# Kernel tuning notes

Hardware: AMD Instinct MI355X
Metric: run time of the kernel (lower is better)

Reference implementation:

```python
import jax, jax.numpy as jnp
import numpy as np

NUM_HEADS = 16
HEAD_DIM = 96          # dim=1536 / 16 heads
ROPE_HALF = HEAD_DIM // 2   # 48 rotary frequencies
FREQ_PER_AXIS = ROPE_HALF // 3  # 16 frequencies per 3D coordinate axis
ROPE_BASE = 10000.0


def _rope_sincos(coords):
    # coords: [B, T, 3] -> sin, cos: [B, T, ROPE_HALF]
    inv_freq = 1.0 / (ROPE_BASE ** (jnp.arange(FREQ_PER_AXIS, dtype=jnp.float32) / FREQ_PER_AXIS))
    # angles per axis: [B, T, 3, F] -> concat axes -> [B, T, 3*F]
    ang = coords[..., :, None] * inv_freq  # [B, T, 3, F]
    ang = ang.reshape(*coords.shape[:-1], ROPE_HALF)
    return jnp.sin(ang), jnp.cos(ang)


def _apply_rotary(x, sin, cos):
    # x: [B, H, T, D]; sin/cos: [B, T, D/2] broadcast over heads
    s = sin[:, None, :, :]
    c = cos[:, None, :, :]
    x1, x2 = x[..., :ROPE_HALF], x[..., ROPE_HALF:]
    return jnp.concatenate([x1 * c - x2 * s, x2 * c + x1 * s], axis=-1)


def setup_inputs() -> dict:
    key = jax.random.key(0)
    ks = jax.random.split(key, 8)
    B, Tq, Tk, D = 2, 1024, 2048, 1536
    std = 1.0 / np.sqrt(D)
    return {
        "x": jax.random.normal(ks[0], (B, Tq, D), jnp.float32),
        "memory": jax.random.normal(ks[1], (B, Tk, D), jnp.float32),
        "query_coords": jax.random.normal(ks[2], (B, Tq, 3), jnp.float32),
        "memory_coords": jax.random.normal(ks[3], (B, Tk, 3), jnp.float32),
        "Wq": jax.random.normal(ks[4], (D, D), jnp.float32) * std,
        "bq": jnp.zeros((D,), jnp.float32),
        "Wk": jax.random.normal(ks[5], (D, D), jnp.float32) * std,
        "bk": jnp.zeros((D,), jnp.float32),
        "Wv": jax.random.normal(ks[6], (D, D), jnp.float32) * std,
        "bv": jnp.zeros((D,), jnp.float32),
        "Wo": jax.random.normal(ks[7], (D, D), jnp.float32) * std,
        "bo": jnp.zeros((D,), jnp.float32),
    }


def reference(x, memory, query_coords, memory_coords, Wq, bq, Wk, bk, Wv, bv, Wo, bo):
    B, Tq, D = x.shape
    Tk = memory.shape[1]
    H, Hd = NUM_HEADS, HEAD_DIM

    # projections (nn.Linear: y = x @ W^T + b)
    q = (jnp.einsum('btd,ed->bte', x, Wq) + bq).reshape(B, Tq, H, Hd).transpose(0, 2, 1, 3)
    k = (jnp.einsum('btd,ed->bte', memory, Wk) + bk).reshape(B, Tk, H, Hd).transpose(0, 2, 1, 3)
    v = (jnp.einsum('btd,ed->bte', memory, Wv) + bv).reshape(B, Tk, H, Hd).transpose(0, 2, 1, 3)

    # 3D-coordinate RoPE (identity augmentation: shift=0, jitter=1, rescale=1)
    q_sin, q_cos = _rope_sincos(query_coords)
    k_sin, k_cos = _rope_sincos(memory_coords)
    q = _apply_rotary(q, q_sin, q_cos)
    k = _apply_rotary(k, k_sin, k_cos)

    # SDPA (standard scaling): softmax(q k^T / sqrt(Hd)) v
    scale = 1.0 / jnp.sqrt(jnp.asarray(Hd, jnp.float32))
    scores = jnp.einsum('bhqd,bhkd->bhqk', q, k) * scale
    attn = jax.nn.softmax(scores, axis=-1)
    out = jnp.einsum('bhqk,bhkd->bhqd', attn, v)  # [B, H, Tq, Hd]

    out = out.transpose(0, 2, 1, 3).reshape(B, Tq, D)
    return jnp.einsum('btd,ed->bte', out, Wo) + bo
```

## Files before the change

### kernel.cpp

```cpp
#include <hip/hip_runtime.h>
#include <math.h>

typedef _Float16 f16;
typedef __attribute__((ext_vector_type(4))) _Float16 f16x4;
typedef __attribute__((ext_vector_type(8))) _Float16 f16x8;
typedef __attribute__((ext_vector_type(4))) float f32x4;
typedef __attribute__((ext_vector_type(16))) float f32x16;

#define NB 2
#define NH 16
#define TQ 1024
#define TK 2048
#define DM 1536
#define HD 96
#define RH 48

__device__ __forceinline__ f32x4 mfma16(f16x8 a, f16x8 b, f32x4 c) {
    return __builtin_amdgcn_mfma_f32_16x16x32_f16(a, b, c, 0, 0, 0);
}

#define GLDS16(gptr, lptr) __builtin_amdgcn_global_load_lds( \
    (const __attribute__((address_space(1))) unsigned int*)(gptr), \
    (__attribute__((address_space(3))) unsigned int*)(lptr), 16, 0, 0)

__global__ void cvt6(const float4* __restrict__ Wq, const float4* __restrict__ Wk,
                     const float4* __restrict__ Wv, const float4* __restrict__ Wo,
                     const float4* __restrict__ X,  const float4* __restrict__ M,
                     f16x4* __restrict__ oq, f16x4* __restrict__ ok,
                     f16x4* __restrict__ ov, f16x4* __restrict__ oo,
                     f16x4* __restrict__ ox, f16x4* __restrict__ om,
                     int nw4, int nx4, int nm4) {
    int i = blockIdx.x * 256 + threadIdx.x;
    const int y = blockIdx.y;
    const int n = (y < 4) ? nw4 : (y == 4 ? nx4 : nm4);
    if (i >= n) return;
    const float4* in = y == 0 ? Wq : y == 1 ? Wk : y == 2 ? Wv : y == 3 ? Wo : y == 4 ? X : M;
    f16x4* out      = y == 0 ? oq : y == 1 ? ok : y == 2 ? ov : y == 3 ? oo : y == 4 ? ox : om;
    float4 v = in[i];
    f16x4 o;
    o[0] = (f16)v.x; o[1] = (f16)v.y; o[2] = (f16)v.z; o[3] = (f16)v.w;
    out[i] = o;
}

__global__ void rope_tab2(const float* __restrict__ cq, const float* __restrict__ cm,
                          float* __restrict__ sq, float* __restrict__ cqo,
                          float* __restrict__ sk, float* __restrict__ cko,
                          int nq, int nk) {
    int i = blockIdx.x * 256 + threadIdx.x;
    int n = blockIdx.y == 0 ? nq : nk;
    if (i >= n) return;
    const float* coords = blockIdx.y == 0 ? cq : cm;
    float* sinT = blockIdx.y == 0 ? sq : sk;
    float* cosT = blockIdx.y == 0 ? cqo : cko;
    int bt = i / 48, idx = i - bt * 48;
    int axis = idx >> 4, f = idx & 15;
    float inv = powf(10000.f, -(float)f * (1.f / 16.f));
    float ang = coords[bt * 3 + axis] * inv;
    sinT[i] = sinf(ang);
    cosT[i] = cosf(ang);
}

__global__ void ropek4(f16* __restrict__ qk, const float* __restrict__ sinT,
                       const float* __restrict__ cosT, int n) {
    int i = blockIdx.x * 256 + threadIdx.x;
    if (i >= n) return;
    int j = i % 12, row = i / 12;
    int p0 = j * 4;
    int t = row & (TK - 1);
    int b = row / (NH * TK);
    long base = (long)row * 128;
    float4 sv = *(const float4*)&sinT[((long)b * TK + t) * 48 + p0];
    float4 cv = *(const float4*)&cosT[((long)b * TK + t) * 48 + p0];
    f16x4 x1 = *(const f16x4*)&qk[base + p0];
    f16x4 x2 = *(const f16x4*)&qk[base + p0 + RH];
    f16x4 o1, o2;
    float s[4] = {sv.x, sv.y, sv.z, sv.w}, c[4] = {cv.x, cv.y, cv.z, cv.w};
#pragma unroll
    for (int e = 0; e < 4; e++) {
        float a = (float)x1[e], bb = (float)x2[e];
        o1[e] = (f16)(a * c[e] - bb * s[e]);
        o2[e] = (f16)(bb * c[e] + a * s[e]);
    }
    *(f16x4*)&qk[base + p0] = o1;
    *(f16x4*)&qk[base + p0 + RH] = o2;
}

__global__ __launch_bounds__(512, 1)
void gemmQKV(const f16* __restrict__ Aq, const f16* __restrict__ Akv,
             const f16* __restrict__ Wqp, const f16* __restrict__ Wkp, const f16* __restrict__ Wvp,
             const float* __restrict__ bqp, const float* __restrict__ bkp, const float* __restrict__ bvp,
             f16* __restrict__ outq, f16* __restrict__ outk, f16* __restrict__ outv) {
    constexpr int MI = 8, NI = 4;
    constexpr int NT = DM / 64;

    __shared__ f16 Buf[2][256 * 64];

    const int tid = threadIdx.x, w = tid >> 6, lane = tid & 63;
    const int l15 = lane & 15, g = lane >> 4;

    int sel = 0, mt, nt;
    const f16* A; const f16* W; const float* bias;
    {
        const int bid = blockIdx.x;
        const int wid = (bid & 7) * 30 + (bid >> 3);
        if (wid < 48)       { sel = 0; mt = wid / 6;        nt = wid - mt * 6;        A = Aq;  W = Wqp; bias = bqp; }
        else if (wid < 144) { sel = 1; int r = wid - 48;  mt = r / 6; nt = r - mt * 6; A = Akv; W = Wkp; bias = bkp; }
        else                { sel = 2; int r = wid - 144; mt = r / 6; nt = r - mt * 6; A = Akv; W = Wvp; bias = bvp; }
    }
    const int m0 = mt * 256, n0 = nt * 256;
    const int wm = (w & 1) * 128;
    const int wn = (w >> 1) * 64;

    int src[4];
#pragma unroll
    for (int r = 0; r < 4; r++) {
        int L = r * 8192 + tid * 16;
        int row = L >> 7, seg = (L >> 4) & 7;
        src[r] = row * DM + ((seg ^ (row & 7)) << 3);
    }
    const f16* Ag = A + (long)m0 * DM;

    int aoff[MI][2];
#pragma unroll
    for (int i = 0; i < MI; i++) {
        int row = wm + i * 16 + l15;
#pragma unroll
        for (int s = 0; s < 2; s++)
            aoff[i][s] = row * 64 + (((s * 4 + g) ^ (row & 7)) << 3);
    }

    const f16* bptr[NI];
#pragma unroll
    for (int j = 0; j < NI; j++)
        bptr[j] = W + (long)(n0 + wn + j * 16 + l15) * DM + g * 8;

#define STG(bufp, kt) do { \
    _Pragma("unroll") for (int r_ = 0; r_ < 4; r_++) \
        GLDS16(Ag + src[r_] + (kt) * 64, &Buf[bufp][r_ * 4096 + w * 512]); \
} while (0)

#define LDB(breg, kt) do { \
    _Pragma("unroll") for (int j_ = 0; j_ < NI; j_++) \
        _Pragma("unroll") for (int s_ = 0; s_ < 2; s_++) \
            breg[j_][s_] = *(const f16x8*)(bptr[j_] + (kt) * 64 + s_ * 32); \
} while (0)

    f32x4 acc[MI][NI] = {};

#define COMPUTE(bufp, breg) do { \
    __builtin_amdgcn_s_setprio(1); \
    _Pragma("unroll") for (int i_ = 0; i_ < MI; i_++) { \
        f16x8 a0 = *(const f16x8*)&Buf[bufp][aoff[i_][0]]; \
        f16x8 a1 = *(const f16x8*)&Buf[bufp][aoff[i_][1]]; \
        _Pragma("unroll") for (int j_ = 0; j_ < NI; j_++) { \
            acc[i_][j_] = mfma16(a0, breg[j_][0], acc[i_][j_]); \
            acc[i_][j_] = mfma16(a1, breg[j_][1], acc[i_][j_]); \
        } \
    } \
    __builtin_amdgcn_s_setprio(0); \
} while (0)

    f16x8 bA[NI][2], bB[NI][2];
    STG(0, 0);
    LDB(bA, 0);

#pragma unroll 1
    for (int t = 0; t < NT; t += 2) {
        if (t + 1 < NT) {
            STG(1, t + 1);
            LDB(bB, t + 1);
            asm volatile("s_waitcnt vmcnt(12)" ::: "memory");
        } else {
            asm volatile("s_waitcnt vmcnt(0)" ::: "memory");
        }
        __builtin_amdgcn_s_barrier();
        __builtin_amdgcn_sched_barrier(0);
        COMPUTE(0, bA);
        __builtin_amdgcn_sched_barrier(0);
        __builtin_amdgcn_s_barrier();
        if (t + 2 < NT) {
            STG(0, t + 2);
            LDB(bA, t + 2);
            asm volatile("s_waitcnt vmcnt(12)" ::: "memory");
        } else {
            asm volatile("s_waitcnt vmcnt(0)" ::: "memory");
        }
        __builtin_amdgcn_s_barrier();
        __builtin_amdgcn_sched_barrier(0);
        COMPUTE(1, bB);
        __builtin_amdgcn_sched_barrier(0);
        __builtin_amdgcn_s_barrier();
    }
#undef STG
#undef LDB
#undef COMPUTE

#pragma unroll
    for (int i = 0; i < MI; i++) {
#pragma unroll
        for (int j = 0; j < NI; j++) {
            const int n = n0 + wn + j * 16 + l15;
            const int mb = m0 + wm + i * 16 + g * 4;
            const int hh = n / HD, hd = n - hh * HD;
            if (sel == 0) {
#pragma unroll
                for (int r = 0; r < 4; r++) {
                    int m = mb + r, bq = m >> 10, t = m & (TQ - 1);
                    outq[(((long)bq * NH + hh) * TQ + t) * 96 + hd] = (f16)(acc[i][j][r] + bias[n]);
                }
            } else if (sel == 1) {
#pragma unroll
                for (int r = 0; r < 4; r++) {
                    int m = mb + r, bq = m >> 11, t = m & (TK - 1);
                    outk[(((long)bq * NH + hh) * TK + t) * 128 + hd] = (f16)(acc[i][j][r] + bias[n]);
                }
            } else {
                int bq = mb >> 11, t = mb & (TK - 1);
                f16x4 pk;
#pragma unroll
                for (int r = 0; r < 4; r++) pk[r] = (f16)(acc[i][j][r] + bias[n]);
                *(f16x4*)&outv[(((long)bq * NH + hh) * HD + hd) * TK + t] = pk;
            }
        }
    }
}

__global__ __launch_bounds__(256, 2)
void gemmO(const f16* __restrict__ A, const f16* __restrict__ W,
           const float* __restrict__ bias, float* __restrict__ outo) {
    constexpr int TPB = 256, MI = 4, NI = 4;
    constexpr int ABUF = 128 * 64;
    constexpr int BUFSZ = 256 * 64;
    constexpr int NT = DM / 64;

    __shared__ f16 Buf[2][BUFSZ];

    const int tid = threadIdx.x, w = tid >> 6, lane = tid & 63;
    const int l15 = lane & 15, g = lane >> 4;
    const int bid = blockIdx.x;
    const int wid = (bid & 7) * 24 + (bid >> 3);
    const int mt = wid / 12, nt = wid - mt * 12;
    const int m0 = mt * 128, n0 = nt * 128;
    const int wm = (w & 1) * 64;
    const int wn = (w >> 1) * 64;

    int src[4];
#pragma unroll
    for (int r = 0; r < 4; r++) {
        int L = r * (TPB * 16) + tid * 16;
        int row = L >> 7, seg = (L >> 4) & 7;
        src[r] = row * DM + ((seg ^ (row & 7)) << 3);
    }
    const f16* Ag = A + (long)m0 * DM;
    const f16* Bg = W + (long)n0 * DM;

    int aoff[MI][2], boff[NI][2];
#pragma unroll
    for (int i = 0; i < MI; i++) {
        int row = wm + i * 16 + l15;
#pragma unroll
        for (int s = 0; s < 2; s++)
            aoff[i][s] = row * 64 + (((s * 4 + g) ^ (row & 7)) << 3);
    }
#pragma unroll
    for (int j = 0; j < NI; j++) {
        int row = wn + j * 16 + l15;
#pragma unroll
        for (int s = 0; s < 2; s++)
            boff[j][s] = ABUF + row * 64 + (((s * 4 + g) ^ (row & 7)) << 3);
    }

#define STG(bufp, kt) do { \
    _Pragma("unroll") for (int r_ = 0; r_ < 4; r_++) { \
        GLDS16(Ag + src[r_] + (kt) * 64, &Buf[bufp][r_ * (TPB * 8) + w * 512]); \
        GLDS16(Bg + src[r_] + (kt) * 64, &Buf[bufp][ABUF + r_ * (TPB * 8) + w * 512]); \
    } \
} while (0)

    f32x4 acc[MI][NI] = {};

#define COMPUTE(bufp) do { \
    f16x8 bf[NI][2]; \
    _Pragma("unroll") for (int j_ = 0; j_ < NI; j_++) \
        _Pragma("unroll") for (int s_ = 0; s_ < 2; s_++) \
            bf[j_][s_] = *(const f16x8*)&Buf[bufp][boff[j_][s_]]; \
    __builtin_amdgcn_s_setprio(1); \
    _Pragma("unroll") for (int i_ = 0; i_ < MI; i_++) { \
        f16x8 a0 = *(const f16x8*)&Buf[bufp][aoff[i_][0]]; \
        f16x8 a1 = *(const f16x8*)&Buf[bufp][aoff[i_][1]]; \
        _Pragma("unroll") for (int j_ = 0; j_ < NI; j_++) { \
            acc[i_][j_] = mfma16(a0, bf[j_][0], acc[i_][j_]); \
            acc[i_][j_] = mfma16(a1, bf[j_][1], acc[i_][j_]); \
        } \
    } \
    __builtin_amdgcn_s_setprio(0); \
} while (0)

    STG(0, 0);
#pragma unroll 1
    for (int t = 0; t < NT; t += 2) {
        STG(1, t + 1);
        asm volatile("s_waitcnt vmcnt(8)" ::: "memory");
        __builtin_amdgcn_s_barrier();
        __builtin_amdgcn_sched_barrier(0);
        COMPUTE(0);
        __builtin_amdgcn_sched_barrier(0);
        __builtin_amdgcn_s_barrier();
        if (t + 2 < NT) {
            STG(0, t + 2);
            asm volatile("s_waitcnt vmcnt(8)" ::: "memory");
        } else {
            asm volatile("s_waitcnt vmcnt(0)" ::: "memory");
        }
        __builtin_amdgcn_s_barrier();
        __builtin_amdgcn_sched_barrier(0);
        COMPUTE(1);
        __builtin_amdgcn_sched_barrier(0);
        __builtin_amdgcn_s_barrier();
    }
#undef STG
#undef COMPUTE

#pragma unroll
    for (int i = 0; i < MI; i++) {
#pragma unroll
        for (int j = 0; j < NI; j++) {
            const int n = n0 + wn + j * 16 + l15;
            const int mb = m0 + wm + i * 16 + g * 4;
#pragma unroll
            for (int r = 0; r < 4; r++)
                outo[(long)(mb + r) * DM + n] = acc[i][j][r] + bias[n];
        }
    }
}

__global__ __launch_bounds__(256, 2) void attn_fwd(
    const f16* __restrict__ Q, const f16* __restrict__ Kg,
    const f16* __restrict__ Vg, const float* __restrict__ sinq,
    const float* __restrict__ cosq, f16* __restrict__ O) {
    __shared__ f16 Kl[2][64 * 128];
    __shared__ f16 Vl[2][96 * 64];
    __shared__ f16 Pl[4][32 * 64];

    const int tid = threadIdx.x, w = tid >> 6, lane = tid & 63;
    const int q31 = lane & 31, hf = lane >> 5;
    const int half = w >> 1, u = w & 1;

    const int linear = blockIdx.x + (int)(gridDim.x * (blockIdx.y + gridDim.y * blockIdx.z));
    const int wid = (linear & 7) * 64 + (linear >> 3);
    const int qc = wid & 15, h = (wid >> 4) & 15, b = wid >> 8;

    const long kbase = (long)(b * NH + h) * TK * 128;
    const long vbase = (long)(b * NH + h) * HD * TK;
    const long qbase = (long)(b * NH + h) * TQ * 96;
    const int q0 = qc * 64 + u * 32;

    int ksrc[8], vsrc[6];
#pragma unroll
    for (int i = 0; i < 8; i++) {
        int L = (u * 8 + i) * 1024 + lane * 16;
        int r = L >> 8, s = (L >> 4) & 15;
        ksrc[i] = r * 128 + ((s ^ (r & 7)) << 3);
    }
#pragma unroll
    for (int i = 0; i < 6; i++) {
        int L = (u * 6 + i) * 1024 + lane * 16;
        int r = L >> 7, s = (L >> 4) & 7;
        vsrc[i] = r * TK + ((s ^ (r & 7)) << 3);
    }

    f16x8 qf[6];
#pragma unroll
    for (int s = 0; s < 6; s++)
        qf[s] = *(const f16x8*)&Q[qbase + (long)(q0 + q31) * 96 + hf * 8 + 16 * s];
    {
        const float QS = 0.10206207261596577f * 1.4426950408889634f;
        const long tb = ((long)b * TQ + q0 + q31) * 48 + hf * 8;
#pragma unroll
        for (int s = 0; s < 3; s++) {
            float4 s0 = *(const float4*)&sinq[tb + 16 * s];
            float4 s1 = *(const float4*)&sinq[tb + 16 * s + 4];
            float4 c0 = *(const float4*)&cosq[tb + 16 * s];
            float4 c1 = *(const float4*)&cosq[tb + 16 * s + 4];
            float sv[8] = {s0.x, s0.y, s0.z, s0.w, s1.x, s1.y, s1.z, s1.w};
            float cv[8] = {c0.x, c0.y, c0.z, c0.w, c1.x, c1.y, c1.z, c1.w};
#pragma unroll
            for (int e = 0; e < 8; e++) {
                float x1 = (float)qf[s][e], x2 = (float)qf[s + 3][e];
                qf[s][e]     = (f16)((x1 * cv[e] - x2 * sv[e]) * QS);
                qf[s + 3][e] = (f16)((x2 * cv[e] + x1 * sv[e]) * QS);
            }
        }
    }

    float mx = -3e38f, ls = 0.f;
    f32x16 acc[3] = {};

#define STAGE(c_) do { \
    const f16* kp_ = Kg + kbase + (long)(half * 16 + (c_)) * (64 * 128); \
    _Pragma("unroll") for (int i_ = 0; i_ < 8; i_++) \
        GLDS16(kp_ + ksrc[i_], &Kl[half][(u * 8 + i_) * 512]); \
    const f16* vp_ = Vg + vbase + (half * 16 + (c_)) * 64; \
    _Pragma("unroll") for (int i_ = 0; i_ < 6; i_++) \
        GLDS16(vp_ + vsrc[i_], &Vl[half][(u * 6 + i_) * 512]); \
} while (0)

    STAGE(0);

    for (int c = 0; c < 16; ++c) {
        __syncthreads();

        f32x16 st[2] = {};
#pragma unroll
        for (int kt = 0; kt < 2; kt++)
#pragma unroll
            for (int s = 0; s < 6; s++) {
                f16x8 kf = *(const f16x8*)&Kl[half][(kt * 32 + q31) * 128 +
                                                    (((hf + 2 * s) ^ (q31 & 7)) << 3)];
                st[kt] = __builtin_amdgcn_mfma_f32_32x32x16_f16(kf, qf[s], st[kt], 0, 0, 0);
            }

        float t16[16];
#pragma unroll
        for (int r = 0; r < 16; r++) t16[r] = fmaxf(st[0][r], st[1][r]);
#pragma unroll
        for (int o = 8; o >= 1; o >>= 1)
#pragma unroll
            for (int r = 0; r < o; r++) t16[r] = fmaxf(t16[r], t16[r + o]);
        float cm = fmaxf(t16[0], __shfl_xor(t16[0], 32));
        float mn = fmaxf(mx, cm);
        float corr = exp2f(mx - mn);
        mx = mn;
#pragma unroll
        for (int kt = 0; kt < 2; kt++)
#pragma unroll
            for (int r = 0; r < 16; r++) st[kt][r] = exp2f(st[kt][r] - mn);
        float s16[16];
#pragma unroll
        for (int r = 0; r < 16; r++) s16[r] = st[0][r] + st[1][r];
#pragma unroll
        for (int o = 8; o >= 1; o >>= 1)
#pragma unroll
            for (int r = 0; r < o; r++) s16[r] += s16[r + o];
        ls = ls * corr + s16[0];
#pragma unroll
        for (int dt = 0; dt < 3; dt++)
#pragma unroll
            for (int r = 0; r < 16; r++) acc[dt][r] *= corr;

#pragma unroll
        for (int kt = 0; kt < 2; kt++)
#pragma unroll
            for (int jq = 0; jq < 4; jq++) {
                f16x4 pk;
#pragma unroll
                for (int e = 0; e < 4; e++) pk[e] = (f16)st[kt][jq * 4 + e];
                int seg = kt * 4 + jq;
                *(f16x4*)&Pl[w][q31 * 64 + ((seg ^ (q31 & 7)) << 3) + hf * 4] = pk;
            }

#pragma unroll
        for (int ks = 0; ks < 4; ks++) {
            f16x8 pf = *(const f16x8*)&Pl[w][q31 * 64 + (((hf + 2 * ks) ^ (q31 & 7)) << 3)];
#pragma unroll
            for (int dt = 0; dt < 3; dt++) {
                f16x8 vf = *(const f16x8*)&Vl[half][(dt * 32 + q31) * 64 +
                                                    (((hf + 2 * ks) ^ (q31 & 7)) << 3)];
                acc[dt] = __builtin_amdgcn_mfma_f32_32x32x16_f16(vf, pf, acc[dt], 0, 0, 0);
            }
        }

        __syncthreads();
        if (c < 15) STAGE(c + 1);
    }

    ls += __shfl_xor(ls, 32);
    float* dump = (float*)&Kl[0][0] + u * (64 * 52);
    __syncthreads();
    if (half == 1) {
        float* dl = dump + lane * 52;
        dl[0] = mx; dl[1] = ls;
#pragma unroll
        for (int dt = 0; dt < 3; dt++)
#pragma unroll
            for (int r = 0; r < 16; r++) dl[2 + dt * 16 + r] = acc[dt][r];
    }
    __syncthreads();
    if (half == 0) {
        const float* dl = dump + lane * 52;
        float mb = dl[0], lsb = dl[1];
        float mf = fmaxf(mx, mb);
        float ca = exp2f(mx - mf), cb = exp2f(mb - mf);
        float inv = 1.f / (ls * ca + lsb * cb);
        const long orow = (long)(b * TQ + q0 + q31) * DM + h * 96;
#pragma unroll
        for (int dt = 0; dt < 3; dt++)
#pragma unroll
            for (int jq = 0; jq < 4; jq++) {
                f16x4 ov;
#pragma unroll
                for (int e = 0; e < 4; e++) {
                    int r = jq * 4 + e;
                    ov[e] = (f16)((acc[dt][r] * ca + dl[2 + dt * 16 + r] * cb) * inv);
                }
                *(f16x4*)&O[orow + dt * 32 + jq * 8 + hf * 4] = ov;
            }
    }
}

extern "C" void kernel_launch(void* const* d_in, const int* in_sizes, int n_in,
                              void* d_out, int out_size, void* d_ws, size_t ws_size,
                              hipStream_t stream) {
    const float* x   = (const float*)d_in[0];
    const float* mem = (const float*)d_in[1];
    const float* qc  = (const float*)d_in[2];
    const float* mc  = (const float*)d_in[3];
    const float* Wq  = (const float*)d_in[4];
    const float* bq  = (const float*)d_in[5];
    const float* Wk  = (const float*)d_in[6];
    const float* bk  = (const float*)d_in[7];
    const float* Wv  = (const float*)d_in[8];
    const float* bv  = (const float*)d_in[9];
    const float* Wo  = (const float*)d_in[10];
    const float* bo  = (const float*)d_in[11];
    float* out = (float*)d_out;

    const long nx  = (long)NB * TQ * DM;
    const long nm  = (long)NB * TK * DM;
    const long nw  = (long)DM * DM;
    const long nq  = (long)NB * NH * TQ * 96;
    const long nkp = (long)NB * NH * TK * 128;
    const long nvt = (long)NB * NH * HD * TK;

    char* ws = (char*)d_ws;
    size_t off = 0;
    auto alloc = [&](size_t bytes) { size_t o = off; off = (off + bytes + 255) & ~(size_t)255; return o; };
    f16* x16   = (f16*)(ws + alloc(nx * 2));
    f16* mem16 = (f16*)(ws + alloc(nm * 2));
    f16* wq16  = (f16*)(ws + alloc(nw * 2));
    f16* wk16  = (f16*)(ws + alloc(nw * 2));
    f16* wv16  = (f16*)(ws + alloc(nw * 2));
    f16* wo16  = (f16*)(ws + alloc(nw * 2));
    f16* q16   = (f16*)(ws + alloc(nq * 2));
    f16* k16p  = (f16*)(ws + alloc(nkp * 2));
    f16* vt16  = (f16*)(ws + alloc(nvt * 2));
    float* sinq = (float*)(ws + alloc((size_t)NB * TQ * 48 * 4));
    float* cosq = (float*)(ws + alloc((size_t)NB * TQ * 48 * 4));
    float* sink = (float*)(ws + alloc((size_t)NB * TK * 48 * 4));
    float* cosk = (float*)(ws + alloc((size_t)NB * TK * 48 * 4));
    f16* at16 = x16;

    cvt6<<<dim3((int)(nm / 4 / 256), 6), 256, 0, stream>>>(
        (const float4*)Wq, (const float4*)Wk, (const float4*)Wv, (const float4*)Wo,
        (const float4*)x, (const float4*)mem,
        (f16x4*)wq16, (f16x4*)wk16, (f16x4*)wv16, (f16x4*)wo16,
        (f16x4*)x16, (f16x4*)mem16,
        (int)(nw / 4), (int)(nx / 4), (int)(nm / 4));

    rope_tab2<<<dim3((NB * TK * 48 + 255) / 256, 2), 256, 0, stream>>>(
        qc, mc, sinq, cosq, sink, cosk, NB * TQ * 48, NB * TK * 48);

    gemmQKV<<<240, 512, 0, stream>>>(
        x16, mem16, wq16, wk16, wv16, bq, bk, bv, q16, k16p, vt16);

    ropek4<<<(NB * NH * TK * 12 + 255) / 256, 256, 0, stream>>>(
        k16p, sink, cosk, NB * NH * TK * 12);

    attn_fwd<<<dim3(16, 16, 2), 256, 0, stream>>>(q16, k16p, vt16, sinq, cosq, at16);

    gemmO<<<192, 256, 0, stream>>>(at16, wo16, bo, out);
}
```

Baseline: 177.7 us.

## Stage weight tiles through LDS and drop double buffering in QKV GEMM

The QKV projection GEMM now loads both the A and W tiles into a single LDS buffer with the same swizzled layout, instead of reading W straight from global memory into registers. The manual double-buffered pipeline with vmcnt waits is replaced by a simple load/sync/compute loop. The launch bounds hint asks for up to four blocks per CU to gain occupancy-based latency hiding. In exchange, global loads no longer overlap with MFMA work inside a block, and two barriers per k-step are added.

```diff
diff --git a/kernel.cpp b/kernel.cpp
--- a/kernel.cpp
+++ b/kernel.cpp
@@ -85,15 +85,16 @@
     *(f16x4*)&qk[base + p0 + RH] = o2;
 }
 
-__global__ __launch_bounds__(512, 1)
+__global__ __launch_bounds__(512, 4)
 void gemmQKV(const f16* __restrict__ Aq, const f16* __restrict__ Akv,
              const f16* __restrict__ Wqp, const f16* __restrict__ Wkp, const f16* __restrict__ Wvp,
              const float* __restrict__ bqp, const float* __restrict__ bkp, const float* __restrict__ bvp,
              f16* __restrict__ outq, f16* __restrict__ outk, f16* __restrict__ outv) {
     constexpr int MI = 8, NI = 4;
+    constexpr int ABUF = 256 * 64;
     constexpr int NT = DM / 64;
 
-    __shared__ f16 Buf[2][256 * 64];
+    __shared__ f16 Buf[2 * 256 * 64];
 
     const int tid = threadIdx.x, w = tid >> 6, lane = tid & 63;
     const int l15 = lane & 15, g = lane >> 4;
@@ -108,19 +109,20 @@
         else                { sel = 2; int r = wid - 144; mt = r / 6; nt = r - mt * 6; A = Akv; W = Wvp; bias = bvp; }
     }
     const int m0 = mt * 256, n0 = nt * 256;
-    const int wm = (w & 1) * 128;
+    const int wm = (w & 1) * (MI * 16);
     const int wn = (w >> 1) * 64;
 
     int src[4];
 #pragma unroll
     for (int r = 0; r < 4; r++) {
-        int L = r * 8192 + tid * 16;
+        int L = r * (512 * 16) + tid * 16;
         int row = L >> 7, seg = (L >> 4) & 7;
         src[r] = row * DM + ((seg ^ (row & 7)) << 3);
     }
     const f16* Ag = A + (long)m0 * DM;
-
-    int aoff[MI][2];
+    const f16* Bg = W + (long)n0 * DM;
+
+    int aoff[MI][2], boff[NI][2];
 #pragma unroll
     for (int i = 0; i < MI; i++) {
         int row = wm + i * 16 + l15;
@@ -128,72 +130,48 @@
         for (int s = 0; s < 2; s++)
             aoff[i][s] = row * 64 + (((s * 4 + g) ^ (row & 7)) << 3);
     }
-
-    const f16* bptr[NI];
-#pragma unroll
-    for (int j = 0; j < NI; j++)
-        bptr[j] = W + (long)(n0 + wn + j * 16 + l15) * DM + g * 8;
-
-#define STG(bufp, kt) do { \
-    _Pragma("unroll") for (int r_ = 0; r_ < 4; r_++) \
-        GLDS16(Ag + src[r_] + (kt) * 64, &Buf[bufp][r_ * 4096 + w * 512]); \
+#pragma unroll
+    for (int j = 0; j < NI; j++) {
+        int row = wn + j * 16 + l15;
+#pragma unroll
+        for (int s = 0; s < 2; s++)
+            boff[j][s] = ABUF + row * 64 + (((s * 4 + g) ^ (row & 7)) << 3);
+    }
+
+#define STG(kt) do { \
+    _Pragma("unroll") for (int r_ = 0; r_ < 4; r_++) { \
+        GLDS16(Ag + src[r_] + (kt) * 64, &Buf[r_ * (512 * 8) + w * 512]); \
+        GLDS16(Bg + src[r_] + (kt) * 64, &Buf[ABUF + r_ * (512 * 8) + w * 512]); \
+    } \
 } while (0)
 
-#define LDB(breg, kt) do { \
-    _Pragma("unroll") for (int j_ = 0; j_ < NI; j_++) \
-        _Pragma("unroll") for (int s_ = 0; s_ < 2; s_++) \
-            breg[j_][s_] = *(const f16x8*)(bptr[j_] + (kt) * 64 + s_ * 32); \
-} while (0)
-
     f32x4 acc[MI][NI] = {};
 
-#define COMPUTE(bufp, breg) do { \
-    __builtin_amdgcn_s_setprio(1); \
-    _Pragma("unroll") for (int i_ = 0; i_ < MI; i_++) { \
-        f16x8 a0 = *(const f16x8*)&Buf[bufp][aoff[i_][0]]; \
-        f16x8 a1 = *(const f16x8*)&Buf[bufp][aoff[i_][1]]; \
-        _Pragma("unroll") for (int j_ = 0; j_ < NI; j_++) { \
-            acc[i_][j_] = mfma16(a0, breg[j_][0], acc[i_][j_]); \
-            acc[i_][j_] = mfma16(a1, breg[j_][1], acc[i_][j_]); \
-        } \
-    } \
-    __builtin_amdgcn_s_setprio(0); \
-} while (0)
-
-    f16x8 bA[NI][2], bB[NI][2];
-    STG(0, 0);
-    LDB(bA, 0);
-
 #pragma unroll 1
-    for (int t = 0; t < NT; t += 2) {
-        if (t + 1 < NT) {
-            STG(1, t + 1);
-            LDB(bB, t + 1);
-            asm volatile("s_waitcnt vmcnt(12)" ::: "memory");
-        } else {
-            asm volatile("s_waitcnt vmcnt(0)" ::: "memory");
+    for (int t = 0; t < NT; ++t) {
+        __syncthreads();
+        STG(t);
+        __syncthreads();
+        f16x8 bf[NI][2];
+#pragma unroll
+        for (int j = 0; j < NI; j++)
+#pragma unroll
+            for (int s = 0; s < 2; s++)
+                bf[j][s] = *(const f16x8*)&Buf[boff[j][s]];
+        __builtin_amdgcn_s_setprio(1);
+#pragma unroll
+        for (int i = 0; i < MI; i++) {
+            f16x8 a0 = *(const f16x8*)&Buf[aoff[i][0]];
+            f16x8 a1 = *(const f16x8*)&Buf[aoff[i][1]];
+#pragma unroll
+            for (int j = 0; j < NI; j++) {
+                acc[i][j] = mfma16(a0, bf[j][0], acc[i][j]);
+                acc[i][j] = mfma16(a1, bf[j][1], acc[i][j]);
+            }
         }
-        __builtin_amdgcn_s_barrier();
-        __builtin_amdgcn_sched_barrier(0);
-        COMPUTE(0, bA);
-        __builtin_amdgcn_sched_barrier(0);
-        __builtin_amdgcn_s_barrier();
-        if (t + 2 < NT) {
-            STG(0, t + 2);
-            LDB(bA, t + 2);
-            asm volatile("s_waitcnt vmcnt(12)" ::: "memory");
-        } else {
-            asm volatile("s_waitcnt vmcnt(0)" ::: "memory");
-        }
-        __builtin_amdgcn_s_barrier();
-        __builtin_amdgcn_sched_barrier(0);
-        COMPUTE(1, bB);
-        __builtin_amdgcn_sched_barrier(0);
-        __builtin_amdgcn_s_barrier();
+        __builtin_amdgcn_s_setprio(0);
     }
 #undef STG
-#undef LDB
-#undef COMPUTE
 
 #pragma unroll
     for (int i = 0; i < MI; i++) {
```

After: 538.4 us. 3.03x slower.
